# Optimization experiments

Hardware: AMD Instinct MI355X
Metric: run time of the kernel (lower is better)

## Reference

```python
import jax, jax.numpy as jnp
import numpy as np

POOL = 7          # cf.pool_size
SR = 2            # roi_align sampling_ratio
LEVELS = [0, 1, 2, 3]
C = 192           # cf.end_filts
HC = 2            # cf.head_classes
RF = 1
N_ROIS = 1000
B = 4


def roi_align_2d(fmap, boxes, batch_inds, pool_size=POOL, sr=SR):
    """Bilinear RoIAlign. fmap [B,C,H,W]; boxes [N,4] = (y1,x1,y2,x2) in fmap pixel coords."""
    _, _, H, W = fmap.shape
    y1, x1, y2, x2 = boxes[:, 0], boxes[:, 1], boxes[:, 2], boxes[:, 3]
    bin_h = jnp.maximum(y2 - y1, 1.0) / pool_size
    bin_w = jnp.maximum(x2 - x1, 1.0) / pool_size
    # sampling offsets within the roi, [pool*sr]
    grid = (jnp.arange(pool_size, dtype=jnp.float32)[:, None]
            + (jnp.arange(sr, dtype=jnp.float32)[None, :] + 0.5) / sr).reshape(-1)
    ys = y1[:, None] + grid[None, :] * bin_h[:, None]   # [N, P*S]
    xs = x1[:, None] + grid[None, :] * bin_w[:, None]   # [N, P*S]
    y = jnp.broadcast_to(ys[:, :, None], (ys.shape[0], ys.shape[1], xs.shape[1]))  # [N,PS,PS]
    x = jnp.broadcast_to(xs[:, None, :], y.shape)
    valid = (y >= -1.0) & (y <= H) & (x >= -1.0) & (x <= W)
    y = jnp.clip(y, 0.0, H - 1)
    x = jnp.clip(x, 0.0, W - 1)
    y0 = jnp.floor(y).astype(jnp.int32)
    x0 = jnp.floor(x).astype(jnp.int32)
    y1i = jnp.minimum(y0 + 1, H - 1)
    x1i = jnp.minimum(x0 + 1, W - 1)
    ly = y - y0
    lx = x - x0
    b = batch_inds[:, None, None]
    f00 = fmap[b, :, y0, x0]    # [N,PS,PS,C]
    f01 = fmap[b, :, y0, x1i]
    f10 = fmap[b, :, y1i, x0]
    f11 = fmap[b, :, y1i, x1i]
    w00 = ((1 - ly) * (1 - lx))[..., None]
    w01 = ((1 - ly) * lx)[..., None]
    w10 = (ly * (1 - lx))[..., None]
    w11 = (ly * lx)[..., None]
    val = (f00 * w00 + f01 * w01 + f10 * w10 + f11 * w11) * valid[..., None]
    n = val.shape[0]
    val = val.reshape(n, pool_size, sr, pool_size, sr, -1).mean(axis=(2, 4))  # [N,P,P,C]
    return jnp.transpose(val, (0, 3, 1, 2))  # [N,C,P,P]


def pyramid_roi_align(fmaps, rois, pool_size=POOL, levels=LEVELS):
    boxes = jax.lax.stop_gradient(rois[:, :4])  # level_boxes.detach() in original
    batch_ix = rois[:, 4].astype(jnp.int32)
    h = boxes[:, 2] - boxes[:, 0]
    w = boxes[:, 3] - boxes[:, 1]
    roi_level = jnp.clip(jnp.round(4.0 + jnp.log2(jnp.sqrt(h * w))),
                         levels[0], levels[-1]).astype(jnp.int32)
    pooled = jnp.zeros((boxes.shape[0], fmaps[0].shape[1], pool_size, pool_size), fmaps[0].dtype)
    for li, lvl in enumerate(levels):
        H, W = fmaps[li].shape[2], fmaps[li].shape[3]
        scale = jnp.asarray([H, W, H, W], jnp.float32)
        p = roi_align_2d(fmaps[li], boxes * scale, batch_ix, pool_size)
        pooled = jnp.where((roi_level == lvl)[:, None, None, None], p, pooled)
    return pooled


def setup_inputs() -> dict:
    key = jax.random.key(0)
    ks = jax.random.split(key, 20)
    fmap0 = jax.random.normal(ks[0], (B, C, 128, 128), jnp.float32)
    fmap1 = jax.random.normal(ks[1], (B, C, 64, 64), jnp.float32)
    fmap2 = jax.random.normal(ks[2], (B, C, 32, 32), jnp.float32)
    fmap3 = jax.random.normal(ks[3], (B, C, 16, 16), jnp.float32)
    # valid normalized rois: (y1,x1,y2,x2,batch_ix)
    cy = jax.random.uniform(ks[4], (N_ROIS,), minval=0.15, maxval=0.85)
    cx = jax.random.uniform(ks[5], (N_ROIS,), minval=0.15, maxval=0.85)
    hh = jax.random.uniform(ks[6], (N_ROIS,), minval=0.02, maxval=0.15)
    hw = jax.random.uniform(ks[7], (N_ROIS,), minval=0.02, maxval=0.15)
    bix = jax.random.randint(ks[8], (N_ROIS,), 0, B).astype(jnp.float32)
    rois = jnp.stack([jnp.clip(cy - hh, 0, 1), jnp.clip(cx - hw, 0, 1),
                      jnp.clip(cy + hh, 0, 1), jnp.clip(cx + hw, 0, 1), bix], axis=1)
    d = C * 4  # 768
    s1 = 1.0 / np.sqrt(C * POOL * POOL)
    s2 = 1.0 / np.sqrt(d)
    params = dict(
        w1=jax.random.normal(ks[9], (d, C, POOL, POOL), jnp.float32) * s1,
        b1=jnp.zeros((d,), jnp.float32),
        w2=jax.random.normal(ks[10], (d, d), jnp.float32) * s2,
        b2=jnp.zeros((d,), jnp.float32),
        w_bbox=jax.random.normal(ks[11], (HC * 4, d), jnp.float32) * s2,
        b_bbox=jnp.zeros((HC * 4,), jnp.float32),
        w_cls=jax.random.normal(ks[12], (HC, d), jnp.float32) * s2,
        b_cls=jnp.zeros((HC,), jnp.float32),
        w_reg=jax.random.normal(ks[13], (HC * RF, d), jnp.float32) * s2,
        b_reg=jnp.zeros((HC * RF,), jnp.float32),
        w_unc=jax.random.normal(ks[14], (HC, d), jnp.float32) * s2,
        b_unc=jnp.zeros((HC,), jnp.float32),
    )
    return dict(fmap0=fmap0, fmap1=fmap1, fmap2=fmap2, fmap3=fmap3, rois=rois, **params)


def reference(fmap0, fmap1, fmap2, fmap3, rois, w1, b1, w2, b2,
              w_bbox, b_bbox, w_cls, b_cls, w_reg, b_reg, w_unc, b_unc):
    x = pyramid_roi_align([fmap0, fmap1, fmap2, fmap3], rois)      # [N,C,7,7]
    x = jax.nn.relu(jnp.einsum('ncij,ocij->no', x, w1) + b1)       # conv1 ks=7 -> 1x1
    x = jax.nn.relu(x @ w2.T + b2)                                 # conv2 1x1
    n = x.shape[0]
    mrcnn_bbox = (x @ w_bbox.T + b_bbox).reshape(n, -1, 4)         # [N,HC,2*dim]
    mrcnn_class_logits = x @ w_cls.T + b_cls                       # [N,HC]
    reg = (x @ w_reg.T + b_reg).reshape(n, -1, RF)
    unc = x @ w_unc.T + b_unc
    mrcnn_regress = jnp.concatenate([reg, unc[..., None]], axis=2)  # [N,HC,RF+1]
    return mrcnn_bbox, mrcnn_class_logits, mrcnn_regress
```

## Files before the change

kernel.cpp:

```cpp
#include <hip/hip_runtime.h>
#include <hip/hip_bf16.h>
#include <cstddef>

typedef __attribute__((ext_vector_type(8))) short short8;
typedef __attribute__((ext_vector_type(16))) float float16;

#define C_CH 192
#define PK   9408
#define D1   768

__device__ __forceinline__ ushort f2bf(float v) {
    return __builtin_bit_cast(unsigned short, __float2bfloat16(v));
}
__device__ __forceinline__ float bf2f(ushort u) {
    return __builtin_bit_cast(float, ((unsigned int)u) << 16);
}

__global__ __launch_bounds__(256) void cvt_bf16(const float* __restrict__ in,
                                                ushort* __restrict__ out, int n4)
{
    int i = blockIdx.x * 256 + threadIdx.x;
    if (i >= n4) return;
    float4 v = ((const float4*)in)[i];
    ushort4 o;
    o.x = f2bf(v.x); o.y = f2bf(v.y); o.z = f2bf(v.z); o.w = f2bf(v.w);
    ((ushort4*)out)[i] = o;
}

__global__ __launch_bounds__(256) void nchw_to_nhwc(
    const float* __restrict__ f0, const float* __restrict__ f1,
    const float* __restrict__ f2, const float* __restrict__ f3,
    ushort* __restrict__ o0, ushort* __restrict__ o1,
    ushort* __restrict__ o2, ushort* __restrict__ o3)
{
    __shared__ float sm[C_CH][33];
    int t = blockIdx.x;
    int b = blockIdx.y;
    const float* in; ushort* out; int HW, hw0;
    if      (t < 512) { in = f0; out = o0; HW = 16384; hw0 = t * 32; }
    else if (t < 640) { in = f1; out = o1; HW = 4096;  hw0 = (t - 512) * 32; }
    else if (t < 672) { in = f2; out = o2; HW = 1024;  hw0 = (t - 640) * 32; }
    else              { in = f3; out = o3; HW = 256;   hw0 = (t - 672) * 32; }

    int tx = threadIdx.x & 31;
    int ty = threadIdx.x >> 5;

    const float* ip = in + (size_t)b * C_CH * HW + hw0;
    #pragma unroll
    for (int c = 0; c < C_CH; c += 8)
        sm[c + ty][tx] = ip[(size_t)(c + ty) * HW + tx];
    __syncthreads();

    ushort* op = out + ((size_t)b * HW + hw0) * C_CH;
    #pragma unroll
    for (int r0 = 0; r0 < 32; r0 += 8) {
        int r = r0 + ty;
        #pragma unroll
        for (int cc = 0; cc < 6; ++cc) {
            int c = cc * 32 + tx;
            op[(size_t)r * C_CH + c] = f2bf(sm[c][r]);
        }
    }
}

__global__ __launch_bounds__(384) void roi_gather(
    const ushort* __restrict__ n0p, const ushort* __restrict__ n1p,
    const ushort* __restrict__ n2p, const ushort* __restrict__ n3p,
    const float* __restrict__ rois, ushort* __restrict__ pooled)
{
    __shared__ int   s_off[196][4];
    __shared__ float s_w[196][4];
    __shared__ ushort s_out[PK];

    const int n   = blockIdx.x;
    const int tid = threadIdx.x;

    float by1 = rois[n*5+0], bx1 = rois[n*5+1];
    float by2 = rois[n*5+2], bx2 = rois[n*5+3];
    int   b   = (int)rois[n*5+4];

    float hh = by2 - by1, ww = bx2 - bx1;
    int lvl = (int)rintf(4.0f + log2f(sqrtf(hh * ww)));
    lvl = min(max(lvl, 0), 3);

    const ushort* fm; int H;
    if      (lvl == 0) { fm = n0p; H = 128; }
    else if (lvl == 1) { fm = n1p; H = 64;  }
    else if (lvl == 2) { fm = n2p; H = 32;  }
    else               { fm = n3p; H = 16;  }
    float Hf = (float)H;

    float y1p = by1 * Hf, x1p = bx1 * Hf;
    float y2p = by2 * Hf, x2p = bx2 * Hf;
    float bin_h = fmaxf(y2p - y1p, 1.0f) * (1.0f / 7.0f);
    float bin_w = fmaxf(x2p - x1p, 1.0f) * (1.0f / 7.0f);

    const ushort* base = fm + (size_t)b * H * H * C_CH;

    if (tid < 196) {
        int s  = tid;
        int sx = s & 1, sy = (s >> 1) & 1, ij = s >> 2;
        int i = ij / 7, j = ij - i * 7;

        float gy = (float)i + 0.25f + 0.5f * (float)sy;
        float y  = y1p + gy * bin_h;
        bool  vy = (y >= -1.0f) && (y <= Hf);
        float yc = fminf(fmaxf(y, 0.0f), Hf - 1.0f);
        int   y0 = (int)floorf(yc);
        float ly = yc - (float)y0;
        int   y1i = min(y0 + 1, H - 1);

        float gx = (float)j + 0.25f + 0.5f * (float)sx;
        float x  = x1p + gx * bin_w;
        bool  vx = (x >= -1.0f) && (x <= Hf);
        float xc = fminf(fmaxf(x, 0.0f), Hf - 1.0f);
        int   x0 = (int)floorf(xc);
        float lx = xc - (float)x0;
        int   x1i = min(x0 + 1, H - 1);

        float vm = (vy && vx) ? 0.25f : 0.0f;
        s_off[s][0] = (y0  * H + x0 ) * C_CH;
        s_off[s][1] = (y0  * H + x1i) * C_CH;
        s_off[s][2] = (y1i * H + x0 ) * C_CH;
        s_off[s][3] = (y1i * H + x1i) * C_CH;
        s_w[s][0] = (1.0f - ly) * (1.0f - lx) * vm;
        s_w[s][1] = (1.0f - ly) * lx * vm;
        s_w[s][2] = ly * (1.0f - lx) * vm;
        s_w[s][3] = ly * lx * vm;
    }
    __syncthreads();

    const int half = tid / C_CH;
    const int c    = tid - half * C_CH;
    const int bin_lo = half * 25;
    const int bin_hi = min(bin_lo + 25, 49);

    for (int bin = bin_lo; bin < bin_hi; ++bin) {
        float acc = 0.0f;
        #pragma unroll
        for (int sub = 0; sub < 4; ++sub) {
            int s = bin * 4 + sub;
            #pragma unroll
            for (int tp = 0; tp < 4; ++tp) {
                int off = __builtin_amdgcn_readfirstlane(s_off[s][tp]);
                float w = s_w[s][tp];
                acc = fmaf(bf2f(base[off + c]), w, acc);
            }
        }
        s_out[c * 49 + bin] = f2bf(acc);
    }
    __syncthreads();

    unsigned int* po = (unsigned int*)(pooled + (size_t)n * PK);
    const unsigned int* so = (const unsigned int*)s_out;
    for (int idx = tid; idx < PK / 2; idx += 384) po[idx] = so[idx];
}

__global__ __launch_bounds__(256) void roi_align_nchw(
    const float* __restrict__ f0, const float* __restrict__ f1,
    const float* __restrict__ f2, const float* __restrict__ f3,
    const float* __restrict__ rois, ushort* __restrict__ pooled, int n_rois)
{
    int idx = blockIdx.x * 256 + threadIdx.x;
    if (idx >= n_rois * PK) return;
    int n  = idx / PK;
    int r  = idx - n * PK;
    int c  = r / 49;
    int ij = r - c * 49;
    int i  = ij / 7;
    int j  = ij - i * 7;

    float by1 = rois[n*5+0], bx1 = rois[n*5+1];
    float by2 = rois[n*5+2], bx2 = rois[n*5+3];
    int   b   = (int)rois[n*5+4];

    float hh = by2 - by1, ww = bx2 - bx1;
    int lvl = (int)rintf(4.0f + log2f(sqrtf(hh * ww)));
    lvl = min(max(lvl, 0), 3);

    const float* fmap; int H;
    if      (lvl == 0) { fmap = f0; H = 128; }
    else if (lvl == 1) { fmap = f1; H = 64;  }
    else if (lvl == 2) { fmap = f2; H = 32;  }
    else               { fmap = f3; H = 16;  }
    float Hf = (float)H;

    float y1p = by1 * Hf, x1p = bx1 * Hf;
    float bin_h = fmaxf(by2 * Hf - y1p, 1.0f) * (1.0f / 7.0f);
    float bin_w = fmaxf(bx2 * Hf - x1p, 1.0f) * (1.0f / 7.0f);

    const float* base = fmap + ((size_t)b * C_CH + c) * (size_t)(H * H);

    float acc = 0.0f;
    #pragma unroll
    for (int sy = 0; sy < 2; ++sy) {
        float y  = y1p + ((float)i + 0.25f + 0.5f * (float)sy) * bin_h;
        bool  vy = (y >= -1.0f) && (y <= Hf);
        float yc = fminf(fmaxf(y, 0.0f), Hf - 1.0f);
        int   y0 = (int)floorf(yc);
        float ly = yc - (float)y0;
        int   y1i = min(y0 + 1, H - 1);
        #pragma unroll
        for (int sx = 0; sx < 2; ++sx) {
            float x  = x1p + ((float)j + 0.25f + 0.5f * (float)sx) * bin_w;
            bool  vx = (x >= -1.0f) && (x <= Hf);
            float xc = fminf(fmaxf(x, 0.0f), Hf - 1.0f);
            int   x0 = (int)floorf(xc);
            float lx = xc - (float)x0;
            int   x1i = min(x0 + 1, H - 1);
            if (vy && vx) {
                float v = base[y0 * H + x0 ] * (1.0f - ly) * (1.0f - lx)
                        + base[y0 * H + x1i] * (1.0f - ly) * lx
                        + base[y1i * H + x0 ] * ly * (1.0f - lx)
                        + base[y1i * H + x1i] * ly * lx;
                acc += v;
            }
        }
    }
    pooled[idx] = f2bf(acc * 0.25f);
}

template<int MODE>
__global__ __launch_bounds__(256) void mfma_gemm(
    const ushort* __restrict__ A, const ushort* __restrict__ W,
    const float* __restrict__ bias, void* __restrict__ outp,
    int M, int N, int K, int nkPer, int nkTotal)
{
    __shared__ char ldsA[2][8192];
    __shared__ char ldsB[2][8192];

    const int t    = threadIdx.x;
    const int lane = t & 63;
    const int wave = t >> 6;
    const int wm = wave >> 1, wn = wave & 1;

    const int m0 = blockIdx.y * 64;
    const int n0 = blockIdx.x * 64;
    const int kb = (MODE == 2) ? blockIdx.z * nkPer : 0;
    const int nk = (MODE == 2) ? min(nkPer, nkTotal - kb) : nkPer;

    const int ks   = t & 3;
    const int mrow = t >> 2;
    const int g    = mrow >> 5;
    const int rw   = mrow & 31;
    const int lof0 = ks*2048 + g*1024 + ((     rw) ^ (ks<<2))*16;
    const int lof1 = ks*2048 + g*1024 + ((32 + rw) ^ (ks<<2))*16;

    const int arow = min(m0 + mrow, M-1);
    const int brow = n0 + mrow;
    const ushort* ap = A + (size_t)arow * K + (size_t)kb * 64 + ks*16;
    const ushort* bp = W + (size_t)brow * K + (size_t)kb * 64 + ks*16;

    float4 ra0, ra1, rb0, rb1;
    float4 qa0, qa1, qb0, qb1;

    ra0 = ((const float4*)ap)[0]; ra1 = ((const float4*)ap)[1];
    rb0 = ((const float4*)bp)[0]; rb1 = ((const float4*)bp)[1];
    *(float4*)&ldsA[0][lof0] = ra0; *(float4*)&ldsA[0][lof1] = ra1;
    *(float4*)&ldsB[0][lof0] = rb0; *(float4*)&ldsB[0][lof1] = rb1;
    {
        int k1 = min(1, nk - 1);
        const ushort* ap1 = ap + (size_t)k1 * 64;
        const ushort* bp1 = bp + (size_t)k1 * 64;
        ra0 = ((const float4*)ap1)[0]; ra1 = ((const float4*)ap1)[1];
        rb0 = ((const float4*)bp1)[0]; rb1 = ((const float4*)bp1)[1];
    }
    __syncthreads();

    float16 acc = {};

    for (int kt = 0; kt < nk; ++kt) {
        {
            int k2 = min(kt + 2, nk - 1);
            const ushort* ap2 = ap + (size_t)k2 * 64;
            const ushort* bp2 = bp + (size_t)k2 * 64;
            qa0 = ((const float4*)ap2)[0]; qa1 = ((const float4*)ap2)[1];
            qb0 = ((const float4*)bp2)[0]; qb1 = ((const float4*)bp2)[1];
        }
        if (kt + 1 < nk) {
            char* dA = ldsA[(kt+1)&1]; char* dB = ldsB[(kt+1)&1];
            *(float4*)&dA[lof0] = ra0; *(float4*)&dA[lof1] = ra1;
            *(float4*)&dB[lof0] = rb0; *(float4*)&dB[lof1] = rb1;
        }
        const char* sA = ldsA[kt&1]; const char* sB = ldsB[kt&1];
        #pragma unroll
        for (int s = 0; s < 4; ++s) {
            int ro = s*2048 + (lane ^ (s<<2))*16;
            short8 af = *(const short8*)&sA[wm*1024 + ro];
            short8 bf = *(const short8*)&sB[wn*1024 + ro];
            acc = __builtin_amdgcn_mfma_f32_32x32x16_bf16(af, bf, acc, 0, 0, 0);
        }
        __syncthreads();
        ra0 = qa0; ra1 = qa1; rb0 = qb0; rb1 = qb1;
    }

    const int col   = lane & 31;
    const int rbase = 4 * (lane >> 5);
    const int nG    = n0 + wn*32 + col;

    if (MODE == 2) {
        float* O = (float*)outp + (size_t)blockIdx.z * M * N;
        #pragma unroll
        for (int r = 0; r < 16; ++r) {
            int row = (r & 3) + 8*(r >> 2) + rbase;
            int mG  = m0 + wm*32 + row;
            if (mG < M) O[(size_t)mG * N + nG] = acc[r];
        }
    } else if (MODE == 1) {
        const float bv = bias[nG];
        ushort* O = (ushort*)outp;
        #pragma unroll
        for (int r = 0; r < 16; ++r) {
            int row = (r & 3) + 8*(r >> 2) + rbase;
            int mG  = m0 + wm*32 + row;
            if (mG < M) O[(size_t)mG * N + nG] = f2bf(fmaxf(acc[r] + bv, 0.0f));
        }
    } else {
        const float bv = bias[nG];
        float* O = (float*)outp;
        #pragma unroll
        for (int r = 0; r < 16; ++r) {
            int row = (r & 3) + 8*(r >> 2) + rbase;
            int mG  = m0 + wm*32 + row;
            if (mG < M) O[(size_t)mG * N + nG] = fmaxf(acc[r] + bv, 0.0f);
        }
    }
}

__global__ __launch_bounds__(256) void reduce_relu_bf16(
    const float* __restrict__ P, const float* __restrict__ bias,
    ushort* __restrict__ Y, int MN, int N, int S)
{
    int idx = blockIdx.x * 256 + threadIdx.x;
    if (idx >= MN / 4) return;
    float4 s = ((const float4*)P)[idx];
    for (int k = 1; k < S; ++k) {
        float4 p = ((const float4*)(P + (size_t)k * MN))[idx];
        s.x += p.x; s.y += p.y; s.z += p.z; s.w += p.w;
    }
    int n4 = idx % (N / 4);
    float4 bv = ((const float4*)bias)[n4];
    ushort4 o;
    o.x = f2bf(fmaxf(s.x + bv.x, 0.0f));
    o.y = f2bf(fmaxf(s.y + bv.y, 0.0f));
    o.z = f2bf(fmaxf(s.z + bv.z, 0.0f));
    o.w = f2bf(fmaxf(s.w + bv.w, 0.0f));
    ((ushort4*)Y)[idx] = o;
}

__global__ __launch_bounds__(256) void reduce_relu_f32(
    const float* __restrict__ P, const float* __restrict__ bias,
    float* __restrict__ Z, int MN, int N, int S)
{
    int idx = blockIdx.x * 256 + threadIdx.x;
    if (idx >= MN / 4) return;
    float4 s = ((const float4*)P)[idx];
    for (int k = 1; k < S; ++k) {
        float4 p = ((const float4*)(P + (size_t)k * MN))[idx];
        s.x += p.x; s.y += p.y; s.z += p.z; s.w += p.w;
    }
    int n4 = idx % (N / 4);
    float4 bv = ((const float4*)bias)[n4];
    float4 o;
    o.x = fmaxf(s.x + bv.x, 0.0f);
    o.y = fmaxf(s.y + bv.y, 0.0f);
    o.z = fmaxf(s.z + bv.z, 0.0f);
    o.w = fmaxf(s.w + bv.w, 0.0f);
    ((float4*)Z)[idx] = o;
}

__global__ __launch_bounds__(256) void heads_kernel(
    const float* __restrict__ Z,
    const float* __restrict__ w_bbox, const float* __restrict__ b_bbox,
    const float* __restrict__ w_cls,  const float* __restrict__ b_cls,
    const float* __restrict__ w_reg,  const float* __restrict__ b_reg,
    const float* __restrict__ w_unc,  const float* __restrict__ b_unc,
    float* __restrict__ out, int n_rois)
{
    int idx = blockIdx.x * 256 + threadIdx.x;
    if (idx >= n_rois * 14) return;
    int n = idx / 14;
    int o = idx - n * 14;

    const float* w; float bb;
    if      (o < 8)  { w = w_bbox + o * D1;        bb = b_bbox[o]; }
    else if (o < 10) { w = w_cls  + (o - 8) * D1;  bb = b_cls[o - 8]; }
    else if (o < 12) { w = w_reg  + (o - 10) * D1; bb = b_reg[o - 10]; }
    else             { w = w_unc  + (o - 12) * D1; bb = b_unc[o - 12]; }

    const float* z = Z + (size_t)n * D1;
    float s = bb;
    for (int k = 0; k < D1; k += 4) {
        float4 zv = *(const float4*)(z + k);
        float4 wv = *(const float4*)(w + k);
        s = fmaf(zv.x, wv.x, s);
        s = fmaf(zv.y, wv.y, s);
        s = fmaf(zv.z, wv.z, s);
        s = fmaf(zv.w, wv.w, s);
    }

    int off;
    int clsOff = n_rois * 8;
    int regOff = n_rois * 8 + n_rois * 2;
    if      (o < 8)  off = n * 8 + o;
    else if (o < 10) off = clsOff + n * 2 + (o - 8);
    else if (o < 12) off = regOff + n * 4 + (o - 10) * 2;
    else             off = regOff + n * 4 + (o - 12) * 2 + 1;
    out[off] = s;
}

extern "C" void kernel_launch(void* const* d_in, const int* in_sizes, int n_in,
                              void* d_out, int out_size, void* d_ws, size_t ws_size,
                              hipStream_t stream)
{
    const float* f0   = (const float*)d_in[0];
    const float* f1   = (const float*)d_in[1];
    const float* f2   = (const float*)d_in[2];
    const float* f3   = (const float*)d_in[3];
    const float* rois = (const float*)d_in[4];
    const float* w1   = (const float*)d_in[5];
    const float* b1   = (const float*)d_in[6];
    const float* w2   = (const float*)d_in[7];
    const float* b2   = (const float*)d_in[8];
    const float* w_bbox = (const float*)d_in[9];
    const float* b_bbox = (const float*)d_in[10];
    const float* w_cls  = (const float*)d_in[11];
    const float* b_cls  = (const float*)d_in[12];
    const float* w_reg  = (const float*)d_in[13];
    const float* b_reg  = (const float*)d_in[14];
    const float* w_unc  = (const float*)d_in[15];
    const float* b_unc  = (const float*)d_in[16];
    float* out = (float*)d_out;

    const int n_rois = in_sizes[4] / 5;
    const int B      = in_sizes[0] / (C_CH * 128 * 128);

    const size_t nh0B = (size_t)B * 16384 * C_CH * 2;
    const size_t nh1B = (size_t)B * 4096  * C_CH * 2;
    const size_t nh2B = (size_t)B * 1024  * C_CH * 2;
    const size_t nh3B = (size_t)B * 256   * C_CH * 2;
    const size_t nhAll = nh0B + nh1B + nh2B + nh3B;
    const size_t poolB = (size_t)n_rois * PK * 2;
    const size_t w1Bb  = (size_t)D1 * PK * 2;
    const size_t w2Bb  = (size_t)D1 * D1 * 2;
    const size_t Yb    = (size_t)n_rois * D1 * 2;
    const size_t Zb    = (size_t)n_rois * D1 * 4;
    const size_t smallB = w2Bb + Yb + Zb;

    const size_t needX = nhAll + poolB + smallB;

    char* ws = (char*)d_ws;

    if (ws_size >= needX) {
        const int SPLIT1 = 5;
        const int SPLIT2 = 2;

        ushort* nh0 = (ushort*)ws;
        ushort* nh1 = nh0 + nh0B/2;
        ushort* nh2 = nh1 + nh1B/2;
        ushort* nh3 = nh2 + nh2B/2;
        ushort* w1B = (ushort*)ws;
        float*  P   = (float*)(ws + w1Bb);
        float*  P2  = (float*)ws;
        ushort* pooledB = (ushort*)(ws + nhAll);
        ushort* w2B = (ushort*)(ws + nhAll + poolB);
        ushort* Y   = w2B + w2Bb/2;
        float*  Z   = (float*)((char*)Y + Yb);

        nchw_to_nhwc<<<dim3(680, B), 256, 0, stream>>>(f0, f1, f2, f3,
                                                       nh0, nh1, nh2, nh3);
        roi_gather<<<n_rois, 384, 0, stream>>>(nh0, nh1, nh2, nh3, rois, pooledB);

        cvt_bf16<<<((D1*PK/4) + 255)/256, 256, 0, stream>>>(w1, w1B, D1*PK/4);
        cvt_bf16<<<((D1*D1/4) + 255)/256, 256, 0, stream>>>(w2, w2B, D1*D1/4);

        {
            int nkTotal = PK / 64;
            int nkPer   = (nkTotal + SPLIT1 - 1) / SPLIT1;
            dim3 grid(D1/64, (n_rois + 63)/64, SPLIT1);
            mfma_gemm<2><<<grid, 256, 0, stream>>>(pooledB, w1B, nullptr, P,
                                                   n_rois, D1, PK, nkPer, nkTotal);
            int MN = n_rois * D1;
            reduce_relu_bf16<<<(MN/4 + 255)/256, 256, 0, stream>>>(P, b1, Y, MN, D1, SPLIT1);
        }
        {
            int nkTotal = D1 / 64;
            int nkPer   = nkTotal / SPLIT2;
            dim3 grid(D1/64, (n_rois + 63)/64, SPLIT2);
            mfma_gemm<2><<<grid, 256, 0, stream>>>(Y, w2B, nullptr, P2,
                                                   n_rois, D1, D1, nkPer, nkTotal);
            int MN = n_rois * D1;
            reduce_relu_f32<<<(MN/4 + 255)/256, 256, 0, stream>>>(P2, b2, Z, MN, D1, SPLIT2);
        }
        heads_kernel<<<(n_rois*14 + 255)/256, 256, 0, stream>>>(
            Z, w_bbox, b_bbox, w_cls, b_cls, w_reg, b_reg, w_unc, b_unc, out, n_rois);
    } else {
        ushort* pooledB = (ushort*)ws;
        ushort* w1B = pooledB + poolB/2;
        ushort* w2B = w1B + w1Bb/2;
        ushort* Y   = w2B + w2Bb/2;
        float*  Z   = (float*)((char*)Y + Yb);

        cvt_bf16<<<((D1*PK/4) + 255)/256, 256, 0, stream>>>(w1, w1B, D1*PK/4);
        cvt_bf16<<<((D1*D1/4) + 255)/256, 256, 0, stream>>>(w2, w2B, D1*D1/4);
        {
            int total = n_rois * PK;
            roi_align_nchw<<<(total + 255)/256, 256, 0, stream>>>(
                f0, f1, f2, f3, rois, pooledB, n_rois);
        }
        {
            dim3 grid(D1/64, (n_rois + 63)/64);
            mfma_gemm<1><<<grid, 256, 0, stream>>>(pooledB, w1B, b1, Y,
                                                   n_rois, D1, PK, PK/64, PK/64);
        }
        {
            dim3 grid(D1/64, (n_rois + 63)/64);
            mfma_gemm<0><<<grid, 256, 0, stream>>>(Y, w2B, b2, Z,
                                                   n_rois, D1, D1, D1/64, D1/64);
        }
        heads_kernel<<<(n_rois*14 + 255)/256, 256, 0, stream>>>(
            Z, w_bbox, b_bbox, w_cls, b_cls, w_reg, b_reg, w_unc, b_unc, out, n_rois);
    }
}
```

Baseline: 274.4 us.

## Vectorize ROI gather loads, merge weight conversions, fuse final reduce with heads

The ROI gather now has each thread load two bf16 channels per 32-bit access, using a wave-uniform scalar base pointer, and splits bins across four groups of 96 threads. The two weight conversion kernels are merged into a single launch. The last split-K reduction, bias and ReLU are fused with the head projections in one kernel, one block per ROI with shuffle reductions. This drops two launches and the Z round trip, at the cost of a less parallel head stage and a layout change to the gather.

```diff
diff --git a/kernel.cpp b/kernel.cpp
--- a/kernel.cpp
+++ b/kernel.cpp
@@ -1,6 +1,7 @@
 #include <hip/hip_runtime.h>
 #include <hip/hip_bf16.h>
 #include <cstddef>
+#include <cstdint>
 
 typedef __attribute__((ext_vector_type(8))) short short8;
 typedef __attribute__((ext_vector_type(16))) float float16;
@@ -14,6 +15,20 @@
 }
 __device__ __forceinline__ float bf2f(ushort u) {
     return __builtin_bit_cast(float, ((unsigned int)u) << 16);
+}
+
+__global__ __launch_bounds__(256) void cvt_bf16_2(
+    const float* __restrict__ in1, ushort* __restrict__ out1, int n4_1,
+    const float* __restrict__ in2, ushort* __restrict__ out2, int n4_2)
+{
+    int i = blockIdx.x * 256 + threadIdx.x;
+    const float* in; ushort* out;
+    if (i < n4_1) { in = in1; out = out1; }
+    else          { i -= n4_1; if (i >= n4_2) return; in = in2; out = out2; }
+    float4 v = ((const float4*)in)[i];
+    ushort4 o;
+    o.x = f2bf(v.x); o.y = f2bf(v.y); o.z = f2bf(v.z); o.w = f2bf(v.w);
+    ((ushort4*)out)[i] = o;
 }
 
 __global__ __launch_bounds__(256) void cvt_bf16(const float* __restrict__ in,
@@ -68,7 +83,7 @@
     const ushort* __restrict__ n2p, const ushort* __restrict__ n3p,
     const float* __restrict__ rois, ushort* __restrict__ pooled)
 {
-    __shared__ int   s_off[196][4];
+    __shared__ int   s_offB[196][4];
     __shared__ float s_w[196][4];
     __shared__ ushort s_out[PK];
 
@@ -95,7 +110,10 @@
     float bin_h = fmaxf(y2p - y1p, 1.0f) * (1.0f / 7.0f);
     float bin_w = fmaxf(x2p - x1p, 1.0f) * (1.0f / 7.0f);
 
-    const ushort* base = fm + (size_t)b * H * H * C_CH;
+    uintptr_t bp = (uintptr_t)(fm + (size_t)b * H * H * C_CH);
+    unsigned int blo = __builtin_amdgcn_readfirstlane((unsigned int)bp);
+    unsigned int bhi = __builtin_amdgcn_readfirstlane((unsigned int)(bp >> 32));
+    const char* sbase = (const char*)((((uintptr_t)bhi) << 32) | blo);
 
     if (tid < 196) {
         int s  = tid;
@@ -119,10 +137,10 @@
         int   x1i = min(x0 + 1, H - 1);
 
         float vm = (vy && vx) ? 0.25f : 0.0f;
-        s_off[s][0] = (y0  * H + x0 ) * C_CH;
-        s_off[s][1] = (y0  * H + x1i) * C_CH;
-        s_off[s][2] = (y1i * H + x0 ) * C_CH;
-        s_off[s][3] = (y1i * H + x1i) * C_CH;
+        s_offB[s][0] = (y0  * H + x0 ) * (C_CH * 2);
+        s_offB[s][1] = (y0  * H + x1i) * (C_CH * 2);
+        s_offB[s][2] = (y1i * H + x0 ) * (C_CH * 2);
+        s_offB[s][3] = (y1i * H + x1i) * (C_CH * 2);
         s_w[s][0] = (1.0f - ly) * (1.0f - lx) * vm;
         s_w[s][1] = (1.0f - ly) * lx * vm;
         s_w[s][2] = ly * (1.0f - lx) * vm;
@@ -130,24 +148,31 @@
     }
     __syncthreads();
 
-    const int half = tid / C_CH;
-    const int c    = tid - half * C_CH;
-    const int bin_lo = half * 25;
-    const int bin_hi = min(bin_lo + 25, 49);
+    const int grp = tid / 96;
+    const int ci  = tid - grp * 96;
+    const int c   = ci * 2;
+    const int c4  = ci * 4;
+    const int bin_lo = grp * 13;
+    const int bin_hi = min(bin_lo + 13, 49);
 
     for (int bin = bin_lo; bin < bin_hi; ++bin) {
-        float acc = 0.0f;
+        float a0 = 0.0f, a1 = 0.0f;
         #pragma unroll
         for (int sub = 0; sub < 4; ++sub) {
             int s = bin * 4 + sub;
             #pragma unroll
             for (int tp = 0; tp < 4; ++tp) {
-                int off = __builtin_amdgcn_readfirstlane(s_off[s][tp]);
+                int ob  = s_offB[s][tp];
                 float w = s_w[s][tp];
-                acc = fmaf(bf2f(base[off + c]), w, acc);
+                unsigned int u = *(const unsigned int*)(sbase + (ob + c4));
+                float lo = __builtin_bit_cast(float, u << 16);
+                float hi = __builtin_bit_cast(float, u & 0xffff0000u);
+                a0 = fmaf(lo, w, a0);
+                a1 = fmaf(hi, w, a1);
             }
         }
-        s_out[c * 49 + bin] = f2bf(acc);
+        s_out[(c + 0) * 49 + bin] = f2bf(a0);
+        s_out[(c + 1) * 49 + bin] = f2bf(a1);
     }
     __syncthreads();
 
@@ -348,25 +373,55 @@
     ((ushort4*)Y)[idx] = o;
 }
 
-__global__ __launch_bounds__(256) void reduce_relu_f32(
-    const float* __restrict__ P, const float* __restrict__ bias,
-    float* __restrict__ Z, int MN, int N, int S)
-{
-    int idx = blockIdx.x * 256 + threadIdx.x;
-    if (idx >= MN / 4) return;
-    float4 s = ((const float4*)P)[idx];
-    for (int k = 1; k < S; ++k) {
-        float4 p = ((const float4*)(P + (size_t)k * MN))[idx];
-        s.x += p.x; s.y += p.y; s.z += p.z; s.w += p.w;
-    }
-    int n4 = idx % (N / 4);
-    float4 bv = ((const float4*)bias)[n4];
-    float4 o;
-    o.x = fmaxf(s.x + bv.x, 0.0f);
-    o.y = fmaxf(s.y + bv.y, 0.0f);
-    o.z = fmaxf(s.z + bv.z, 0.0f);
-    o.w = fmaxf(s.w + bv.w, 0.0f);
-    ((float4*)Z)[idx] = o;
+__global__ __launch_bounds__(256) void reduce_heads(
+    const float* __restrict__ P2, const float* __restrict__ b2, int S, int MN,
+    const float* __restrict__ w_bbox, const float* __restrict__ b_bbox,
+    const float* __restrict__ w_cls,  const float* __restrict__ b_cls,
+    const float* __restrict__ w_reg,  const float* __restrict__ b_reg,
+    const float* __restrict__ w_unc,  const float* __restrict__ b_unc,
+    float* __restrict__ out, int n_rois)
+{
+    __shared__ float zrow[D1];
+    const int m   = blockIdx.x;
+    const int tid = threadIdx.x;
+
+    const float* Pm = P2 + (size_t)m * D1;
+    #pragma unroll
+    for (int r = 0; r < 3; ++r) {
+        int k = r * 256 + tid;
+        float v = Pm[k];
+        for (int s = 1; s < S; ++s) v += Pm[(size_t)s * MN + k];
+        zrow[k] = fmaxf(v + b2[k], 0.0f);
+    }
+    __syncthreads();
+
+    const int wave = tid >> 6;
+    const int lane = tid & 63;
+    for (int o = wave; o < 14; o += 4) {
+        const float* w; float bb;
+        if      (o < 8)  { w = w_bbox + o * D1;        bb = b_bbox[o]; }
+        else if (o < 10) { w = w_cls  + (o - 8) * D1;  bb = b_cls[o - 8]; }
+        else if (o < 12) { w = w_reg  + (o - 10) * D1; bb = b_reg[o - 10]; }
+        else             { w = w_unc  + (o - 12) * D1; bb = b_unc[o - 12]; }
+        float p = 0.0f;
+        #pragma unroll
+        for (int r = 0; r < 12; ++r) {
+            int k = r * 64 + lane;
+            p = fmaf(zrow[k], w[k], p);
+        }
+        #pragma unroll
+        for (int d = 32; d >= 1; d >>= 1) p += __shfl_down(p, d, 64);
+        if (lane == 0) {
+            int off;
+            int clsOff = n_rois * 8;
+            int regOff = n_rois * 10;
+            if      (o < 8)  off = m * 8 + o;
+            else if (o < 10) off = clsOff + m * 2 + (o - 8);
+            else if (o < 12) off = regOff + m * 4 + (o - 10) * 2;
+            else             off = regOff + m * 4 + (o - 12) * 2 + 1;
+            out[off] = p + bb;
+        }
+    }
 }
 
 __global__ __launch_bounds__(256) void heads_kernel(
@@ -401,7 +456,7 @@
 
     int off;
     int clsOff = n_rois * 8;
-    int regOff = n_rois * 8 + n_rois * 2;
+    int regOff = n_rois * 10;
     if      (o < 8)  off = n * 8 + o;
     else if (o < 10) off = clsOff + n * 2 + (o - 8);
     else if (o < 12) off = regOff + n * 4 + (o - 10) * 2;
@@ -465,15 +520,16 @@
         ushort* pooledB = (ushort*)(ws + nhAll);
         ushort* w2B = (ushort*)(ws + nhAll + poolB);
         ushort* Y   = w2B + w2Bb/2;
-        float*  Z   = (float*)((char*)Y + Yb);
 
         nchw_to_nhwc<<<dim3(680, B), 256, 0, stream>>>(f0, f1, f2, f3,
                                                        nh0, nh1, nh2, nh3);
         roi_gather<<<n_rois, 384, 0, stream>>>(nh0, nh1, nh2, nh3, rois, pooledB);
 
-        cvt_bf16<<<((D1*PK/4) + 255)/256, 256, 0, stream>>>(w1, w1B, D1*PK/4);
-        cvt_bf16<<<((D1*D1/4) + 255)/256, 256, 0, stream>>>(w2, w2B, D1*D1/4);
-
+        {
+            int n41 = D1*PK/4, n42 = D1*D1/4;
+            cvt_bf16_2<<<(n41 + n42 + 255)/256, 256, 0, stream>>>(
+                w1, w1B, n41, w2, w2B, n42);
+        }
         {
             int nkTotal = PK / 64;
             int nkPer   = (nkTotal + SPLIT1 - 1) / SPLIT1;
@@ -490,10 +546,9 @@
             mfma_gemm<2><<<grid, 256, 0, stream>>>(Y, w2B, nullptr, P2,
                                                    n_rois, D1, D1, nkPer, nkTotal);
             int MN = n_rois * D1;
-            reduce_relu_f32<<<(MN/4 + 255)/256, 256, 0, stream>>>(P2, b2, Z, MN, D1, SPLIT2);
-        }
-        heads_kernel<<<(n_rois*14 + 255)/256, 256, 0, stream>>>(
-            Z, w_bbox, b_bbox, w_cls, b_cls, w_reg, b_reg, w_unc, b_unc, out, n_rois);
+            reduce_heads<<<n_rois, 256, 0, stream>>>(P2, b2, SPLIT2, MN,
+                w_bbox, b_bbox, w_cls, b_cls, w_reg, b_reg, w_unc, b_unc, out, n_rois);
+        }
     } else {
         ushort* pooledB = (ushort*)ws;
         ushort* w1B = pooledB + poolB/2;
```

Result: faster. 246.2 us (-10.3%).
